# Kernel tuning notes

Measured on AMD Instinct MI355X. Metric: run time of the kernel, lower is better.

The kernel has to match this reference:

```python
import jax, jax.numpy as jnp
import numpy as np

K_HOP = 2

def _graph_conv(x, A, W, b):
    feats = [x]
    xk = x
    for _ in range(K_HOP):
        xk = jnp.einsum('bmn,bnc->bmc', A, xk)
        feats.append(xk)
    return jnp.concatenate(feats, -1) @ W + b

def _pair_mlp(y, W2, b2, W1, b1, shape):
    # normal_conv: fc1(relu(fc2(y))).reshape(shape)
    return (jax.nn.relu(y @ W2 + b2) @ W1 + b1).reshape(shape)

def setup_inputs():
    key = jax.random.key(0)
    ks = jax.random.split(key, 16)
    B, T, N = 8, 12, 200
    C_IN, H, D, H_ST = 2, 64, 32, 64
    def lin(k, fi, fo):
        k1, k2 = jax.random.split(k)
        s = 1.0 / float(np.sqrt(fi))
        return (jax.random.uniform(k1, (fi, fo), jnp.float32, -s, s),
                jax.random.uniform(k2, (fo,), jnp.float32, -s, s))
    W_s2d, b_s2d = lin(ks[0], H_ST, D)
    W_rz, b_rz = lin(ks[1], 1 + D, 2 * D)
    W_h, b_h = lin(ks[2], 1 + D, D)
    Wc2, bc2 = lin(ks[3], 2 * D, D)
    Wc1, bc1 = lin(ks[4], D, 1)
    Wm2, bm2 = lin(ks[5], 2 * D, D)
    Wm1, bm1 = lin(ks[6], D, 1)
    gin = (C_IN + H) * (1 + K_HOP)
    W_ru, b_ru = lin(ks[7], gin, 2 * H)
    W_cand, b_cand = lin(ks[8], gin, H)
    Wp1, bp1 = lin(ks[9], H, H)
    Wp2, bp2 = lin(ks[10], H, 1)
    x = jax.random.normal(ks[11], (B, T, N, C_IN), jnp.float32)
    node_fea_st = jax.random.normal(ks[12], (N, H_ST), jnp.float32)
    return dict(x=x, node_fea_st=node_fea_st, W_s2d=W_s2d, b_s2d=b_s2d,
                W_rz=W_rz, b_rz=b_rz, W_h=W_h, b_h=b_h,
                Wc2=Wc2, bc2=bc2, Wc1=Wc1, bc1=bc1,
                Wm2=Wm2, bm2=bm2, Wm1=Wm1, bm1=bm1,
                W_ru=W_ru, b_ru=b_ru, W_cand=W_cand, b_cand=b_cand,
                Wp1=Wp1, bp1=bp1, Wp2=Wp2, bp2=bp2)

def reference(x, node_fea_st, W_s2d, b_s2d, W_rz, b_rz, W_h, b_h,
              Wc2, bc2, Wc1, bc1, Wm2, bm2, Wm1, bm1,
              W_ru, b_ru, W_cand, b_cand, Wp1, bp1, Wp2, bp2):
    B, T, N, _ = x.shape
    H = W_cand.shape[1]
    D = W_h.shape[1]
    # states_dy init: linear_s2d(node_fea_st) broadcast over batch
    state_dy0 = jnp.broadcast_to((node_fea_st @ W_s2d + b_s2d)[None], (B, N, D))
    state0 = jnp.zeros((B, N, H), x.dtype)
    xs = jnp.transpose(x, (1, 0, 2, 3))  # [T,B,N,C]

    def step(carry, xt):
        state, state_dy = carry
        inp1 = xt[..., :1]
        # DynamicGraphGRU (conv_method='normal')
        rz = jax.nn.sigmoid(jnp.concatenate([inp1, state_dy], -1) @ W_rz + b_rz)
        r, z = jnp.split(rz, 2, -1)
        h = jnp.tanh(jnp.concatenate([inp1, r * state_dy], -1) @ W_h + b_h)
        new_dy = z * state_dy + (1.0 - z) * h
        s = jax.nn.relu(new_dy)  # [B,N,D]
        y = jnp.concatenate([jnp.broadcast_to(s[:, :, None, :], (B, N, N, D)),
                             jnp.broadcast_to(s[:, None, :, :], (B, N, N, D))], -1)
        g = _pair_mlp(y, Wc2, bc2, Wc1, bc1, (B, N, N))
        m = _pair_mlp(y, Wm2, bm2, Wm1, bm1, (B, N, N))
        A = g * jax.nn.sigmoid(m)  # dynamic graph [B,N,N]
        # DCGRUCell with supports=[A]
        ru = jax.nn.sigmoid(_graph_conv(jnp.concatenate([xt, state], -1), A, W_ru, b_ru))
        rr, u = jnp.split(ru, 2, -1)
        c = jnp.tanh(_graph_conv(jnp.concatenate([xt, rr * state], -1), A, W_cand, b_cand))
        new_state = u * state + (1.0 - u) * c
        return (new_state, new_dy), A

    (state, _), dy_graphs = jax.lax.scan(step, (state0, state_dy0), xs)
    # predictor: Linear -> LeakyReLU -> Linear
    pred = jax.nn.leaky_relu(state @ Wp1 + bp1) @ Wp2 + bp2  # [B,N,1]
    return pred, dy_graphs
```

## Files before the change

kernel.cpp:

```cpp
#include <hip/hip_runtime.h>
#include <math.h>

#define B_ 8
#define T_ 12
#define N_ 200
#define R_ 1600
#define NN_ 40000

__device__ __forceinline__ float sigm(float v) { return 1.f / (1.f + expf(-v)); }

__global__ void __launch_bounds__(256) k_dyall(
        const float* __restrict__ x,  const float* __restrict__ nf,
        const float* __restrict__ Ws2d, const float* __restrict__ bs2d,
        const float* __restrict__ Wrz,  const float* __restrict__ brz,
        const float* __restrict__ Wh,   const float* __restrict__ bh,
        const float* __restrict__ Wc2,  const float* __restrict__ Wm2,
        const float* __restrict__ bc2,  const float* __restrict__ bm2,
        float* __restrict__ Pc, float* __restrict__ Qc,
        float* __restrict__ Pm, float* __restrict__ Qm,
        float* __restrict__ state) {
    __shared__ float sWs2d[64 * 32], sWrz[33 * 64], sWh[33 * 32];
    __shared__ float sWc2[64 * 32], sWm2[64 * 32];
    __shared__ float sbrz[64], sbh[32], sbs2d[32], sbc2[32], sbm2[32];
    __shared__ float nfs[4][64], dy[4][32], in1[4][33], in2[4][33], rz[4][64], s4[4][32];
    int bk = blockIdx.x, tid = threadIdx.x;
    int w = tid >> 6, o = tid & 63;
    int row = bk * 4 + w, b = row / N_, n = row % N_;
    state[bk * 256 + tid] = 0.f;
    for (int idx = tid; idx < 2048; idx += 256) sWs2d[idx] = Ws2d[idx];
    for (int idx = tid; idx < 2112; idx += 256) sWrz[idx] = Wrz[idx];
    for (int idx = tid; idx < 1056; idx += 256) sWh[idx] = Wh[idx];
    for (int idx = tid; idx < 2048; idx += 256) { sWc2[idx] = Wc2[idx]; sWm2[idx] = Wm2[idx]; }
    if (tid < 64) sbrz[tid] = brz[tid];
    if (tid < 32) { sbh[tid] = bh[tid]; sbs2d[tid] = bs2d[tid];
                    sbc2[tid] = bc2[tid]; sbm2[tid] = bm2[tid]; }
    nfs[w][o] = nf[n * 64 + o];
    __syncthreads();
    if (o < 32) {
        float acc = sbs2d[o];
        #pragma unroll 8
        for (int i = 0; i < 64; ++i) acc += nfs[w][i] * sWs2d[i * 32 + o];
        dy[w][o] = acc;
    }
    __syncthreads();
    for (int t = 0; t < T_; ++t) {
        if (o == 0) { float v = x[((b * T_ + t) * N_ + n) * 2]; in1[w][0] = v; in2[w][0] = v; }
        if (o < 32) in1[w][o + 1] = dy[w][o];
        __syncthreads();
        float acc = sbrz[o];
        #pragma unroll
        for (int i = 0; i < 33; ++i) acc += in1[w][i] * sWrz[i * 64 + o];
        rz[w][o] = sigm(acc);
        __syncthreads();
        if (o < 32) in2[w][o + 1] = rz[w][o] * dy[w][o];
        __syncthreads();
        if (o < 32) {
            float h = sbh[o];
            #pragma unroll
            for (int i = 0; i < 33; ++i) h += in2[w][i] * sWh[i * 32 + o];
            h = tanhf(h);
            float z = rz[w][32 + o];
            float nd = z * dy[w][o] + (1.f - z) * h;
            dy[w][o] = nd;
            s4[w][o] = nd > 0.f ? nd : 0.f;
        }
        __syncthreads();
        size_t base = ((size_t)t * R_ + row) * 32;
        for (int idx = o; idx < 128; idx += 64) {
            int mat = idx >> 5, k = idx & 31;
            const float* W = (mat < 2) ? sWc2 : sWm2;
            int rb = (mat & 1) ? 32 : 0;
            float a = (mat == 0) ? sbc2[k] : (mat == 2) ? sbm2[k] : 0.f;
            #pragma unroll
            for (int i = 0; i < 32; ++i) a += s4[w][i] * W[(rb + i) * 32 + k];
            ((mat == 0) ? Pc : (mat == 1) ? Qc : (mat == 2) ? Pm : Qm)[base + k] = a;
        }
        __syncthreads();
    }
}

__global__ void __launch_bounds__(256) k_pairall(
        const float* __restrict__ Pc, const float* __restrict__ Qc,
        const float* __restrict__ Pm, const float* __restrict__ Qm,
        const float* __restrict__ Wc1, const float* __restrict__ bc1,
        const float* __restrict__ Wm1, const float* __restrict__ bm1,
        float* __restrict__ out) {
    __shared__ float sPc[16][36], sQc[16][36], sPm[16][36], sQm[16][36];
    __shared__ float sWc1[32], sWm1[32];
    int z = blockIdx.z;
    int i0 = blockIdx.x * 16, j0 = blockIdx.y * 16;
    int tid = threadIdx.y * 16 + threadIdx.x;
    size_t tb = (size_t)z * N_;
    for (int l = tid; l < 128; l += 256) {
        int r = l >> 3, q = l & 7;
        int gi = i0 + r, gj = j0 + r;
        float4 z4 = make_float4(0.f, 0.f, 0.f, 0.f);
        *(float4*)&sPc[r][4 * q] = (gi < N_) ? *(const float4*)&Pc[(tb + gi) * 32 + 4 * q] : z4;
        *(float4*)&sPm[r][4 * q] = (gi < N_) ? *(const float4*)&Pm[(tb + gi) * 32 + 4 * q] : z4;
        *(float4*)&sQc[r][4 * q] = (gj < N_) ? *(const float4*)&Qc[(tb + gj) * 32 + 4 * q] : z4;
        *(float4*)&sQm[r][4 * q] = (gj < N_) ? *(const float4*)&Qm[(tb + gj) * 32 + 4 * q] : z4;
    }
    if (tid < 32) { sWc1[tid] = Wc1[tid]; sWm1[tid] = Wm1[tid]; }
    __syncthreads();
    int i = i0 + threadIdx.y, j = j0 + threadIdx.x;
    if (i >= N_ || j >= N_) return;
    int ty = threadIdx.y, tx = threadIdx.x;
    float g0 = 0.f, g1 = 0.f, m0 = 0.f, m1 = 0.f;
    #pragma unroll
    for (int kg = 0; kg < 8; ++kg) {
        float4 pc = *(const float4*)&sPc[ty][4 * kg];
        float4 qc = *(const float4*)&sQc[tx][4 * kg];
        float4 wc = *(const float4*)&sWc1[4 * kg];
        g0 += fmaxf(pc.x + qc.x, 0.f) * wc.x + fmaxf(pc.y + qc.y, 0.f) * wc.y;
        g1 += fmaxf(pc.z + qc.z, 0.f) * wc.z + fmaxf(pc.w + qc.w, 0.f) * wc.w;
        float4 pm = *(const float4*)&sPm[ty][4 * kg];
        float4 qm = *(const float4*)&sQm[tx][4 * kg];
        float4 wm = *(const float4*)&sWm1[4 * kg];
        m0 += fmaxf(pm.x + qm.x, 0.f) * wm.x + fmaxf(pm.y + qm.y, 0.f) * wm.y;
        m1 += fmaxf(pm.z + qm.z, 0.f) * wm.z + fmaxf(pm.w + qm.w, 0.f) * wm.w;
    }
    float g = g0 + g1 + bc1[0];
    float m = m0 + m1 + bm1[0];
    out[R_ + (((size_t)z * N_ + i) * N_ + j)] = g * sigm(m);
}

__global__ void __launch_bounds__(256) k_a2(
        const float* __restrict__ Abase, float* __restrict__ Cbase, int nmat) {
    __shared__ float Ast[32][132];
    __shared__ float Bs[32][68];
    int bx = blockIdx.x;
    int z = bx % nmat, tl = bx / nmat;
    int i0 = (tl >> 2) * 128, j0 = (tl & 3) * 64;
    const float* Az = Abase + (size_t)z * NN_;
    float* Cz = Cbase + (size_t)z * NN_;
    int tid = threadIdx.x;
    int tx = tid & 15, ty = tid >> 4;
    float acc[8][4] = {};
    for (int k0 = 0; k0 < 200; k0 += 32) {
        {
            int i = tid >> 1;
            int kb = (tid & 1) * 16;
            int gi = i0 + i;
            #pragma unroll
            for (int q = 0; q < 4; ++q) {
                int k = kb + q * 4;
                int gk = k0 + k;
                float4 v = make_float4(0.f, 0.f, 0.f, 0.f);
                if (gi < N_) {
                    if (gk + 3 < N_) v = *(const float4*)&Az[gi * N_ + gk];
                    else {
                        float t0 = (gk + 0 < N_) ? Az[gi * N_ + gk + 0] : 0.f;
                        float t1 = (gk + 1 < N_) ? Az[gi * N_ + gk + 1] : 0.f;
                        float t2 = (gk + 2 < N_) ? Az[gi * N_ + gk + 2] : 0.f;
                        float t3 = (gk + 3 < N_) ? Az[gi * N_ + gk + 3] : 0.f;
                        v = make_float4(t0, t1, t2, t3);
                    }
                }
                Ast[k + 0][i] = v.x; Ast[k + 1][i] = v.y;
                Ast[k + 2][i] = v.z; Ast[k + 3][i] = v.w;
            }
        }
        {
            #pragma unroll
            for (int q = 0; q < 2; ++q) {
                int id = tid + 256 * q;
                int k = id >> 4, jq = (id & 15) * 4;
                int gk = k0 + k, gj = j0 + jq;
                float4 v = make_float4(0.f, 0.f, 0.f, 0.f);
                if (gk < N_) {
                    if (gj + 3 < N_) v = *(const float4*)&Az[gk * N_ + gj];
                    else {
                        float t0 = (gj + 0 < N_) ? Az[gk * N_ + gj + 0] : 0.f;
                        float t1 = (gj + 1 < N_) ? Az[gk * N_ + gj + 1] : 0.f;
                        float t2 = (gj + 2 < N_) ? Az[gk * N_ + gj + 2] : 0.f;
                        float t3 = (gj + 3 < N_) ? Az[gk * N_ + gj + 3] : 0.f;
                        v = make_float4(t0, t1, t2, t3);
                    }
                }
                *(float4*)&Bs[k][jq] = v;
            }
        }
        __syncthreads();
        #pragma unroll 8
        for (int k = 0; k < 32; ++k) {
            float4 a0 = *(const float4*)&Ast[k][ty * 8];
            float4 a1 = *(const float4*)&Ast[k][ty * 8 + 4];
            float4 bv = *(const float4*)&Bs[k][tx * 4];
            acc[0][0] += a0.x * bv.x; acc[0][1] += a0.x * bv.y; acc[0][2] += a0.x * bv.z; acc[0][3] += a0.x * bv.w;
            acc[1][0] += a0.y * bv.x; acc[1][1] += a0.y * bv.y; acc[1][2] += a0.y * bv.z; acc[1][3] += a0.y * bv.w;
            acc[2][0] += a0.z * bv.x; acc[2][1] += a0.z * bv.y; acc[2][2] += a0.z * bv.z; acc[2][3] += a0.z * bv.w;
            acc[3][0] += a0.w * bv.x; acc[3][1] += a0.w * bv.y; acc[3][2] += a0.w * bv.z; acc[3][3] += a0.w * bv.w;
            acc[4][0] += a1.x * bv.x; acc[4][1] += a1.x * bv.y; acc[4][2] += a1.x * bv.z; acc[4][3] += a1.x * bv.w;
            acc[5][0] += a1.y * bv.x; acc[5][1] += a1.y * bv.y; acc[5][2] += a1.y * bv.z; acc[5][3] += a1.y * bv.w;
            acc[6][0] += a1.z * bv.x; acc[6][1] += a1.z * bv.y; acc[6][2] += a1.z * bv.z; acc[6][3] += a1.z * bv.w;
            acc[7][0] += a1.w * bv.x; acc[7][1] += a1.w * bv.y; acc[7][2] += a1.w * bv.z; acc[7][3] += a1.w * bv.w;
        }
        __syncthreads();
    }
    #pragma unroll
    for (int r = 0; r < 8; ++r) {
        int gi = i0 + ty * 8 + r;
        if (gi >= N_) continue;
        int gj = j0 + tx * 4;
        if (gj + 3 < N_) {
            *(float4*)&Cz[gi * N_ + gj] = make_float4(acc[r][0], acc[r][1], acc[r][2], acc[r][3]);
        } else {
            #pragma unroll
            for (int e = 0; e < 4; ++e) if (gj + e < N_) Cz[gi * N_ + gj + e] = acc[r][e];
        }
    }
}

__global__ void __launch_bounds__(256) k_xh(
        const float* __restrict__ Abase, const float* __restrict__ A2base,
        const float* __restrict__ x, int z0, float* __restrict__ xh) {
    __shared__ float xtl[400];
    int zl = blockIdx.x, tid = threadIdx.x;
    int z = z0 + zl, t = z >> 3, b = z & 7;
    int w = tid >> 6, l = tid & 63;
    const float* xb = x + ((size_t)(b * T_ + t)) * N_ * 2;
    for (int idx = tid; idx < 400; idx += 256) xtl[idx] = xb[idx];
    __syncthreads();
    for (int it = 0; it < 50; ++it) {
        int i = it * 4 + w;
        float p0 = 0.f, p1 = 0.f, p2 = 0.f, p3 = 0.f;
        if (l < 50) {
            float4 a4 = *(const float4*)(Abase + (size_t)zl * NN_ + i * 200 + 4 * l);
            float4 c4 = *(const float4*)(A2base + (size_t)zl * NN_ + i * 200 + 4 * l);
            #pragma unroll
            for (int q = 0; q < 4; ++q) {
                float av = (&a4.x)[q], cv = (&c4.x)[q];
                float x0 = xtl[(4 * l + q) * 2], x1 = xtl[(4 * l + q) * 2 + 1];
                p0 += av * x0; p1 += av * x1; p2 += cv * x0; p3 += cv * x1;
            }
        }
        #pragma unroll
        for (int off = 32; off > 0; off >>= 1) {
            p0 += __shfl_down(p0, off); p1 += __shfl_down(p1, off);
            p2 += __shfl_down(p2, off); p3 += __shfl_down(p3, off);
        }
        if (l == 0) *(float4*)(xh + ((size_t)zl * N_ + i) * 4) = make_float4(p0, p1, p2, p3);
    }
}

__global__ void __launch_bounds__(256) k_ru2(
        const float* __restrict__ At, const float* __restrict__ A2t,
        const float* __restrict__ xht,
        const float* __restrict__ x, int t, const float* __restrict__ state,
        const float* __restrict__ Wru, const float* __restrict__ bru,
        float* __restrict__ rs, float* __restrict__ ub) {
    __shared__ float a2s[2 * 200], c2s[2 * 200];
    __shared__ float hpA[4][64], hpC[4][64];
    __shared__ float g8[2][132];
    __shared__ float xts[4];
    int bx = blockIdx.x;
    int b = bx & 7, i0 = (bx >> 3) * 2;
    int tid = threadIdx.x;
    const float* F = state + (size_t)b * (N_ * 64);
    {
        const float4* Ar = (const float4*)(At + ((size_t)b * N_ + i0) * 200);
        const float4* Cr = (const float4*)(A2t + ((size_t)b * N_ + i0) * 200);
        if (tid < 100) { ((float4*)a2s)[tid] = Ar[tid]; ((float4*)c2s)[tid] = Cr[tid]; }
        if (tid >= 128 && tid < 132) {
            int l = tid - 128;
            xts[l] = x[((size_t)(b * T_ + t) * N_ + i0 + (l >> 1)) * 2 + (l & 1)];
        }
        if (tid >= 136 && tid < 144) {
            int l = tid - 136, rr = l >> 2, q = l & 3;
            g8[rr][(q < 2) ? q : q + 64] = xht[((size_t)b * N_ + i0 + rr) * 4 + q];
        }
    }
    __syncthreads();
    {
        int w = tid >> 6, lane = tid & 63;
        int r = w & 1, h = w >> 1;
        int cg = lane & 15, jq = lane >> 4;
        const float* ar = a2s + r * 200 + h * 100;
        const float* cr = c2s + r * 200 + h * 100;
        const float* Fb = F + (size_t)(h * 100) * 64 + 4 * cg;
        float4 accA = make_float4(0.f, 0.f, 0.f, 0.f);
        float4 accC = make_float4(0.f, 0.f, 0.f, 0.f);
        #pragma unroll 5
        for (int m = 0; m < 25; ++m) {
            int j = jq + 4 * m;
            float av = ar[j], cv = cr[j];
            float4 f4 = *(const float4*)&Fb[(size_t)j * 64];
            accA.x += av * f4.x; accA.y += av * f4.y; accA.z += av * f4.z; accA.w += av * f4.w;
            accC.x += cv * f4.x; accC.y += cv * f4.y; accC.z += cv * f4.z; accC.w += cv * f4.w;
        }
        accA.x += __shfl_xor(accA.x, 16); accA.y += __shfl_xor(accA.y, 16);
        accA.z += __shfl_xor(accA.z, 16); accA.w += __shfl_xor(accA.w, 16);
        accC.x += __shfl_xor(accC.x, 16); accC.y += __shfl_xor(accC.y, 16);
        accC.z += __shfl_xor(accC.z, 16); accC.w += __shfl_xor(accC.w, 16);
        accA.x += __shfl_xor(accA.x, 32); accA.y += __shfl_xor(accA.y, 32);
        accA.z += __shfl_xor(accA.z, 32); accA.w += __shfl_xor(accA.w, 32);
        accC.x += __shfl_xor(accC.x, 32); accC.y += __shfl_xor(accC.y, 32);
        accC.z += __shfl_xor(accC.z, 32); accC.w += __shfl_xor(accC.w, 32);
        if (lane < 16) {
            *(float4*)&hpA[w][4 * cg] = accA;
            *(float4*)&hpC[w][4 * cg] = accC;
        }
    }
    __syncthreads();
    {
        int mt = tid >> 7, r = (tid >> 6) & 1, c = tid & 63;
        float v = mt ? (hpC[r][c] + hpC[2 + r][c]) : (hpA[r][c] + hpA[2 + r][c]);
        g8[r][(mt ? 68 : 2) + c] = v;
    }
    __syncthreads();
    {
        int rq = tid >> 7, c = tid & 127;
        int grow = i0 + rq;
        const float* Fr = F + (size_t)grow * 64;
        float a0 = bru[c] + xts[rq * 2 + 0] * Wru[c] + xts[rq * 2 + 1] * Wru[128 + c];
        #pragma unroll 4
        for (int kg = 0; kg < 16; ++kg) {
            float4 f0 = *(const float4*)&Fr[4 * kg];
            const float* Wp = Wru + (size_t)(2 + 4 * kg) * 128 + c;
            a0 += f0.x * Wp[0] + f0.y * Wp[128] + f0.z * Wp[256] + f0.w * Wp[384];
        }
        #pragma unroll 4
        for (int kg = 0; kg < 33; ++kg) {
            float4 f0 = *(const float4*)&g8[rq][4 * kg];
            const float* Wp = Wru + (size_t)(66 + 4 * kg) * 128 + c;
            a0 += f0.x * Wp[0] + f0.y * Wp[128] + f0.z * Wp[256] + f0.w * Wp[384];
        }
        float v = sigm(a0);
        size_t go = (size_t)b * N_ + grow;
        if (c < 64) rs[go * 64 + c] = v * Fr[c];
        else        ub[go * 64 + (c - 64)] = v;
    }
}

__global__ void __launch_bounds__(256) k_cand2(
        const float* __restrict__ At, const float* __restrict__ A2t,
        const float* __restrict__ xht,
        const float* __restrict__ x, int t, const float* __restrict__ rsin,
        const float* __restrict__ Wcd, const float* __restrict__ bcd,
        const float* __restrict__ ub, float* __restrict__ state) {
    __shared__ float a2s[2 * 200], c2s[2 * 200];
    __shared__ float hpA[4][64], hpC[4][64];
    __shared__ float g8[2][132];
    __shared__ float xts[4];
    __shared__ float gp[2][2][64];
    int bx = blockIdx.x;
    int b = bx & 7, i0 = (bx >> 3) * 2;
    int tid = threadIdx.x;
    const float* F = rsin + (size_t)b * (N_ * 64);
    {
        const float4* Ar = (const float4*)(At + ((size_t)b * N_ + i0) * 200);
        const float4* Cr = (const float4*)(A2t + ((size_t)b * N_ + i0) * 200);
        if (tid < 100) { ((float4*)a2s)[tid] = Ar[tid]; ((float4*)c2s)[tid] = Cr[tid]; }
        if (tid >= 128 && tid < 132) {
            int l = tid - 128;
            xts[l] = x[((size_t)(b * T_ + t) * N_ + i0 + (l >> 1)) * 2 + (l & 1)];
        }
        if (tid >= 136 && tid < 144) {
            int l = tid - 136, rr = l >> 2, q = l & 3;
            g8[rr][(q < 2) ? q : q + 64] = xht[((size_t)b * N_ + i0 + rr) * 4 + q];
        }
    }
    __syncthreads();
    {
        int w = tid >> 6, lane = tid & 63;
        int r = w & 1, h = w >> 1;
        int cg = lane & 15, jq = lane >> 4;
        const float* ar = a2s + r * 200 + h * 100;
        const float* cr = c2s + r * 200 + h * 100;
        const float* Fb = F + (size_t)(h * 100) * 64 + 4 * cg;
        float4 accA = make_float4(0.f, 0.f, 0.f, 0.f);
        float4 accC = make_float4(0.f, 0.f, 0.f, 0.f);
        #pragma unroll 5
        for (int m = 0; m < 25; ++m) {
            int j = jq + 4 * m;
            float av = ar[j], cv = cr[j];
            float4 f4 = *(const float4*)&Fb[(size_t)j * 64];
            accA.x += av * f4.x; accA.y += av * f4.y; accA.z += av * f4.z; accA.w += av * f4.w;
            accC.x += cv * f4.x; accC.y += cv * f4.y; accC.z += cv * f4.z; accC.w += cv * f4.w;
        }
        accA.x += __shfl_xor(accA.x, 16); accA.y += __shfl_xor(accA.y, 16);
        accA.z += __shfl_xor(accA.z, 16); accA.w += __shfl_xor(accA.w, 16);
        accC.x += __shfl_xor(accC.x, 16); accC.y += __shfl_xor(accC.y, 16);
        accC.z += __shfl_xor(accC.z, 16); accC.w += __shfl_xor(accC.w, 16);
        accA.x += __shfl_xor(accA.x, 32); accA.y += __shfl_xor(accA.y, 32);
        accA.z += __shfl_xor(accA.z, 32); accA.w += __shfl_xor(accA.w, 32);
        accC.x += __shfl_xor(accC.x, 32); accC.y += __shfl_xor(accC.y, 32);
        accC.z += __shfl_xor(accC.z, 32); accC.w += __shfl_xor(accC.w, 32);
        if (lane < 16) {
            *(float4*)&hpA[w][4 * cg] = accA;
            *(float4*)&hpC[w][4 * cg] = accC;
        }
    }
    __syncthreads();
    {
        int mt = tid >> 7, r = (tid >> 6) & 1, c = tid & 63;
        float v = mt ? (hpC[r][c] + hpC[2 + r][c]) : (hpA[r][c] + hpA[2 + r][c]);
        g8[r][(mt ? 68 : 2) + c] = v;
    }
    __syncthreads();
    {
        int kh = tid >> 7, rq = (tid >> 6) & 1, c = tid & 63;
        int grow = i0 + rq;
        const float* Fr = F + (size_t)grow * 64;
        float a0 = 0.f;
        if (kh == 0) {
            a0 = bcd[c] + xts[rq * 2 + 0] * Wcd[c] + xts[rq * 2 + 1] * Wcd[64 + c];
            #pragma unroll 4
            for (int kg = 0; kg < 16; ++kg) {
                float4 f0 = *(const float4*)&Fr[4 * kg];
                const float* Wp = Wcd + (size_t)(2 + 4 * kg) * 64 + c;
                a0 += f0.x * Wp[0] + f0.y * Wp[64] + f0.z * Wp[128] + f0.w * Wp[192];
            }
            #pragma unroll 4
            for (int kg = 0; kg < 8; ++kg) {
                float4 f0 = *(const float4*)&g8[rq][4 * kg];
                const float* Wp = Wcd + (size_t)(66 + 4 * kg) * 64 + c;
                a0 += f0.x * Wp[0] + f0.y * Wp[64] + f0.z * Wp[128] + f0.w * Wp[192];
            }
        } else {
            #pragma unroll 5
            for (int kg = 8; kg < 33; ++kg) {
                float4 f0 = *(const float4*)&g8[rq][4 * kg];
                const float* Wp = Wcd + (size_t)(66 + 4 * kg) * 64 + c;
                a0 += f0.x * Wp[0] + f0.y * Wp[64] + f0.z * Wp[128] + f0.w * Wp[192];
            }
        }
        gp[kh][rq][c] = a0;
    }
    __syncthreads();
    if (tid < 128) {
        int rq = tid >> 6, c = tid & 63;
        size_t go = (size_t)b * N_ + i0 + rq;
        float a = gp[0][rq][c] + gp[1][rq][c];
        float cnd = tanhf(a);
        float u = ub[go * 64 + c];
        float st = state[go * 64 + c];
        state[go * 64 + c] = u * st + (1.f - u) * cnd;
    }
}

__global__ void __launch_bounds__(64) k_pred(
        const float* __restrict__ state,
        const float* __restrict__ Wp1, const float* __restrict__ bp1,
        const float* __restrict__ Wp2, const float* __restrict__ bp2,
        float* __restrict__ out) {
    __shared__ float st[64];
    int row = blockIdx.x;
    int tid = threadIdx.x;
    st[tid] = state[row * 64 + tid];
    __syncthreads();
    float acc = bp1[tid];
    #pragma unroll 8
    for (int a = 0; a < 64; ++a) acc += st[a] * Wp1[a * 64 + tid];
    acc = acc > 0.f ? acc : 0.01f * acc;
    float v = acc * Wp2[tid];
    #pragma unroll
    for (int off = 32; off > 0; off >>= 1) v += __shfl_down(v, off);
    if (tid == 0) out[row] = v + bp2[0];
}

extern "C" void kernel_launch(void* const* d_in, const int* in_sizes, int n_in,
                              void* d_out, int out_size, void* d_ws, size_t ws_size,
                              hipStream_t stream) {
    const float* x    = (const float*)d_in[0];
    const float* nf   = (const float*)d_in[1];
    const float* Ws2d = (const float*)d_in[2];
    const float* bs2d = (const float*)d_in[3];
    const float* Wrz  = (const float*)d_in[4];
    const float* brz  = (const float*)d_in[5];
    const float* Wh   = (const float*)d_in[6];
    const float* bh   = (const float*)d_in[7];
    const float* Wc2  = (const float*)d_in[8];
    const float* bc2  = (const float*)d_in[9];
    const float* Wc1  = (const float*)d_in[10];
    const float* bc1  = (const float*)d_in[11];
    const float* Wm2  = (const float*)d_in[12];
    const float* bm2  = (const float*)d_in[13];
    const float* Wm1  = (const float*)d_in[14];
    const float* bm1  = (const float*)d_in[15];
    const float* Wru  = (const float*)d_in[16];
    const float* bru  = (const float*)d_in[17];
    const float* Wcand= (const float*)d_in[18];
    const float* bcand= (const float*)d_in[19];
    const float* Wp1  = (const float*)d_in[20];
    const float* bp1  = (const float*)d_in[21];
    const float* Wp2  = (const float*)d_in[22];
    const float* bp2  = (const float*)d_in[23];
    float* out = (float*)d_out;

    float* ws = (float*)d_ws;
    const size_t PQ = (size_t)T_ * R_ * 32;
    float* Pc = ws;
    float* Qc = Pc + PQ;
    float* Pm = Qc + PQ;
    float* Qm = Pm + PQ;

    const size_t A2F = (size_t)96 * NN_;
    const size_t XHF = (size_t)96 * N_ * 4;
    const size_t FULL_NEED = (A2F + XHF + 3 * (size_t)R_ * 64) * 4;
    bool full = ws_size >= FULL_NEED;

    const float* Aall = out + R_;

    if (full) {
        float* A2base = ws;
        float* xhbase = ws + A2F;
        float* state  = xhbase + XHF;
        float* rs     = state + (size_t)R_ * 64;
        float* ub     = rs + (size_t)R_ * 64;

        k_dyall<<<400, 256, 0, stream>>>(x, nf, Ws2d, bs2d, Wrz, brz, Wh, bh,
                                         Wc2, Wm2, bc2, bm2, Pc, Qc, Pm, Qm, state);
        k_pairall<<<dim3(13, 13, 96), dim3(16, 16), 0, stream>>>(
            Pc, Qc, Pm, Qm, Wc1, bc1, Wm1, bm1, out);
        k_a2<<<96 * 8, 256, 0, stream>>>(Aall, A2base, 96);
        k_xh<<<96, 256, 0, stream>>>(Aall, A2base, x, 0, xhbase);

        for (int t = 0; t < T_; ++t) {
            const float* At  = Aall + (size_t)t * 8 * NN_;
            const float* A2t = A2base + (size_t)t * 8 * NN_;
            const float* xht = xhbase + (size_t)t * 8 * N_ * 4;
            k_ru2  <<<800, 256, 0, stream>>>(At, A2t, xht, x, t, state, Wru, bru, rs, ub);
            k_cand2<<<800, 256, 0, stream>>>(At, A2t, xht, x, t, rs, Wcand, bcand, ub, state);
        }
        k_pred<<<R_, 64, 0, stream>>>(state, Wp1, bp1, Wp2, bp2, out);
    } else {
        float* A2base = ws + 4 * PQ;
        float* xhbase = A2base + (size_t)8 * NN_;
        float* state  = xhbase + (size_t)8 * N_ * 4;
        float* rs     = state + (size_t)R_ * 64;
        float* ub     = rs + (size_t)R_ * 64;

        k_dyall<<<400, 256, 0, stream>>>(x, nf, Ws2d, bs2d, Wrz, brz, Wh, bh,
                                         Wc2, Wm2, bc2, bm2, Pc, Qc, Pm, Qm, state);
        k_pairall<<<dim3(13, 13, 96), dim3(16, 16), 0, stream>>>(
            Pc, Qc, Pm, Qm, Wc1, bc1, Wm1, bm1, out);
        for (int t = 0; t < T_; ++t) {
            const float* At = Aall + (size_t)t * 8 * NN_;
            k_a2<<<8 * 8, 256, 0, stream>>>(At, A2base, 8);
            k_xh<<<8, 256, 0, stream>>>(At, A2base, x, t * 8, xhbase);
            k_ru2  <<<800, 256, 0, stream>>>(At, A2base, xhbase, x, t, state, Wru, bru, rs, ub);
            k_cand2<<<800, 256, 0, stream>>>(At, A2base, xhbase, x, t, rs, Wcand, bcand, ub, state);
        }
        k_pred<<<R_, 64, 0, stream>>>(state, Wp1, bp1, Wp2, bp2, out);
    }
}
```

Measured before the change: 550.8 us.

## Split gate linear layers across K with shared feature staging and float4 weight loads

The ru and candidate kernels now build a contiguous 198-wide feature row per node in shared memory (x, state, A·F, A²·F) instead of mixing global and shared reads. The output linear is then split along the reduction dimension across thread groups, with each thread loading float4 weight vectors and computing both rows, followed by a shared-memory partial-sum reduction. This replaces long serial per-thread dot products with strided scalar weight loads, aiming to cut latency and reuse each weight load for two rows. In exchange it adds an extra barrier, more shared memory, and a partial-sum reduction step.

```diff
diff --git a/kernel.cpp b/kernel.cpp
--- a/kernel.cpp
+++ b/kernel.cpp
@@ -251,8 +251,8 @@
         float* __restrict__ rs, float* __restrict__ ub) {
     __shared__ float a2s[2 * 200], c2s[2 * 200];
     __shared__ float hpA[4][64], hpC[4][64];
-    __shared__ float g8[2][132];
-    __shared__ float xts[4];
+    __shared__ float feat[2][200];
+    __shared__ float gp[8][2][128];
     int bx = blockIdx.x;
     int b = bx & 7, i0 = (bx >> 3) * 2;
     int tid = threadIdx.x;
@@ -261,13 +261,17 @@
         const float4* Ar = (const float4*)(At + ((size_t)b * N_ + i0) * 200);
         const float4* Cr = (const float4*)(A2t + ((size_t)b * N_ + i0) * 200);
         if (tid < 100) { ((float4*)a2s)[tid] = Ar[tid]; ((float4*)c2s)[tid] = Cr[tid]; }
-        if (tid >= 128 && tid < 132) {
-            int l = tid - 128;
-            xts[l] = x[((size_t)(b * T_ + t) * N_ + i0 + (l >> 1)) * 2 + (l & 1)];
-        }
-        if (tid >= 136 && tid < 144) {
-            int l = tid - 136, rr = l >> 2, q = l & 3;
-            g8[rr][(q < 2) ? q : q + 64] = xht[((size_t)b * N_ + i0 + rr) * 4 + q];
+        if (tid >= 100 && tid < 164) {
+            int l = tid - 100, r = l >> 5, q = l & 31;
+            *(float2*)&feat[r][2 + 2 * q] = *(const float2*)&F[(size_t)(i0 + r) * 64 + 2 * q];
+        }
+        if (tid >= 164 && tid < 168) {
+            int l = tid - 164;
+            feat[l >> 1][l & 1] = x[((size_t)(b * T_ + t) * N_ + i0 + (l >> 1)) * 2 + (l & 1)];
+        }
+        if (tid >= 168 && tid < 176) {
+            int l = tid - 168, rr = l >> 2, q = l & 3;
+            feat[rr][(q < 2) ? (66 + q) : (132 + q - 2)] = xht[((size_t)b * N_ + i0 + rr) * 4 + q];
         }
     }
     __syncthreads();
@@ -305,29 +309,32 @@
     {
         int mt = tid >> 7, r = (tid >> 6) & 1, c = tid & 63;
         float v = mt ? (hpC[r][c] + hpC[2 + r][c]) : (hpA[r][c] + hpA[2 + r][c]);
-        g8[r][(mt ? 68 : 2) + c] = v;
+        feat[r][(mt ? 134 : 68) + c] = v;
+    }
+    __syncthreads();
+    {
+        int cq = tid & 31, kh = tid >> 5;
+        int k0 = 25 * kh, kend = (k0 + 25 < 198) ? (k0 + 25) : 198;
+        float4 s0 = make_float4(0.f, 0.f, 0.f, 0.f);
+        float4 s1 = make_float4(0.f, 0.f, 0.f, 0.f);
+        for (int k = k0; k < kend; ++k) {
+            float4 w4 = *(const float4*)&Wru[(size_t)k * 128 + 4 * cq];
+            float f0 = feat[0][k], f1 = feat[1][k];
+            s0.x += f0 * w4.x; s0.y += f0 * w4.y; s0.z += f0 * w4.z; s0.w += f0 * w4.w;
+            s1.x += f1 * w4.x; s1.y += f1 * w4.y; s1.z += f1 * w4.z; s1.w += f1 * w4.w;
+        }
+        *(float4*)&gp[kh][0][4 * cq] = s0;
+        *(float4*)&gp[kh][1][4 * cq] = s1;
     }
     __syncthreads();
     {
         int rq = tid >> 7, c = tid & 127;
-        int grow = i0 + rq;
-        const float* Fr = F + (size_t)grow * 64;
-        float a0 = bru[c] + xts[rq * 2 + 0] * Wru[c] + xts[rq * 2 + 1] * Wru[128 + c];
-        #pragma unroll 4
-        for (int kg = 0; kg < 16; ++kg) {
-            float4 f0 = *(const float4*)&Fr[4 * kg];
-            const float* Wp = Wru + (size_t)(2 + 4 * kg) * 128 + c;
-            a0 += f0.x * Wp[0] + f0.y * Wp[128] + f0.z * Wp[256] + f0.w * Wp[384];
-        }
-        #pragma unroll 4
-        for (int kg = 0; kg < 33; ++kg) {
-            float4 f0 = *(const float4*)&g8[rq][4 * kg];
-            const float* Wp = Wru + (size_t)(66 + 4 * kg) * 128 + c;
-            a0 += f0.x * Wp[0] + f0.y * Wp[128] + f0.z * Wp[256] + f0.w * Wp[384];
-        }
-        float v = sigm(a0);
-        size_t go = (size_t)b * N_ + grow;
-        if (c < 64) rs[go * 64 + c] = v * Fr[c];
+        float a = bru[c];
+        #pragma unroll
+        for (int h = 0; h < 8; ++h) a += gp[h][rq][c];
+        float v = sigm(a);
+        size_t go = (size_t)b * N_ + i0 + rq;
+        if (c < 64) rs[go * 64 + c] = v * feat[rq][2 + c];
         else        ub[go * 64 + (c - 64)] = v;
     }
 }
@@ -340,9 +347,8 @@
         const float* __restrict__ ub, float* __restrict__ state) {
     __shared__ float a2s[2 * 200], c2s[2 * 200];
     __shared__ float hpA[4][64], hpC[4][64];
-    __shared__ float g8[2][132];
-    __shared__ float xts[4];
-    __shared__ float gp[2][2][64];
+    __shared__ float feat[2][200];
+    __shared__ float gp[16][2][64];
     int bx = blockIdx.x;
     int b = bx & 7, i0 = (bx >> 3) * 2;
     int tid = threadIdx.x;
@@ -351,13 +357,17 @@
         const float4* Ar = (const float4*)(At + ((size_t)b * N_ + i0) * 200);
         const float4* Cr = (const float4*)(A2t + ((size_t)b * N_ + i0) * 200);
         if (tid < 100) { ((float4*)a2s)[tid] = Ar[tid]; ((float4*)c2s)[tid] = Cr[tid]; }
-        if (tid >= 128 && tid < 132) {
-            int l = tid - 128;
-            xts[l] = x[((size_t)(b * T_ + t) * N_ + i0 + (l >> 1)) * 2 + (l & 1)];
-        }
-        if (tid >= 136 && tid < 144) {
-            int l = tid - 136, rr = l >> 2, q = l & 3;
-            g8[rr][(q < 2) ? q : q + 64] = xht[((size_t)b * N_ + i0 + rr) * 4 + q];
+        if (tid >= 100 && tid < 164) {
+            int l = tid - 100, r = l >> 5, q = l & 31;
+            *(float2*)&feat[r][2 + 2 * q] = *(const float2*)&F[(size_t)(i0 + r) * 64 + 2 * q];
+        }
+        if (tid >= 164 && tid < 168) {
+            int l = tid - 164;
+            feat[l >> 1][l & 1] = x[((size_t)(b * T_ + t) * N_ + i0 + (l >> 1)) * 2 + (l & 1)];
+        }
+        if (tid >= 168 && tid < 176) {
+            int l = tid - 168, rr = l >> 2, q = l & 3;
+            feat[rr][(q < 2) ? (66 + q) : (132 + q - 2)] = xht[((size_t)b * N_ + i0 + rr) * 4 + q];
         }
     }
     __syncthreads();
@@ -395,43 +405,30 @@
     {
         int mt = tid >> 7, r = (tid >> 6) & 1, c = tid & 63;
         float v = mt ? (hpC[r][c] + hpC[2 + r][c]) : (hpA[r][c] + hpA[2 + r][c]);
-        g8[r][(mt ? 68 : 2) + c] = v;
-    }
-    __syncthreads();
-    {
-        int kh = tid >> 7, rq = (tid >> 6) & 1, c = tid & 63;
-        int grow = i0 + rq;
-        const float* Fr = F + (size_t)grow * 64;
-        float a0 = 0.f;
-        if (kh == 0) {
-            a0 = bcd[c] + xts[rq * 2 + 0] * Wcd[c] + xts[rq * 2 + 1] * Wcd[64 + c];
-            #pragma unroll 4
-            for (int kg = 0; kg < 16; ++kg) {
-                float4 f0 = *(const float4*)&Fr[4 * kg];
-                const float* Wp = Wcd + (size_t)(2 + 4 * kg) * 64 + c;
-                a0 += f0.x * Wp[0] + f0.y * Wp[64] + f0.z * Wp[128] + f0.w * Wp[192];
-            }
-            #pragma unroll 4
-            for (int kg = 0; kg < 8; ++kg) {
-                float4 f0 = *(const float4*)&g8[rq][4 * kg];
-                const float* Wp = Wcd + (size_t)(66 + 4 * kg) * 64 + c;
-                a0 += f0.x * Wp[0] + f0.y * Wp[64] + f0.z * Wp[128] + f0.w * Wp[192];
-            }
-        } else {
-            #pragma unroll 5
-            for (int kg = 8; kg < 33; ++kg) {
-                float4 f0 = *(const float4*)&g8[rq][4 * kg];
-                const float* Wp = Wcd + (size_t)(66 + 4 * kg) * 64 + c;
-                a0 += f0.x * Wp[0] + f0.y * Wp[64] + f0.z * Wp[128] + f0.w * Wp[192];
-            }
-        }
-        gp[kh][rq][c] = a0;
+        feat[r][(mt ? 134 : 68) + c] = v;
+    }
+    __syncthreads();
+    {
+        int cq = tid & 15, kh = tid >> 4;
+        int k0 = 13 * kh, kend = (k0 + 13 < 198) ? (k0 + 13) : 198;
+        float4 s0 = make_float4(0.f, 0.f, 0.f, 0.f);
+        float4 s1 = make_float4(0.f, 0.f, 0.f, 0.f);
+        for (int k = k0; k < kend; ++k) {
+            float4 w4 = *(const float4*)&Wcd[(size_t)k * 64 + 4 * cq];
+            float f0 = feat[0][k], f1 = feat[1][k];
+            s0.x += f0 * w4.x; s0.y += f0 * w4.y; s0.z += f0 * w4.z; s0.w += f0 * w4.w;
+            s1.x += f1 * w4.x; s1.y += f1 * w4.y; s1.z += f1 * w4.z; s1.w += f1 * w4.w;
+        }
+        *(float4*)&gp[kh][0][4 * cq] = s0;
+        *(float4*)&gp[kh][1][4 * cq] = s1;
     }
     __syncthreads();
     if (tid < 128) {
         int rq = tid >> 6, c = tid & 63;
+        float a = bcd[c];
+        #pragma unroll
+        for (int h = 0; h < 16; ++h) a += gp[h][rq][c];
         size_t go = (size_t)b * N_ + i0 + rq;
-        float a = gp[0][rq][c] + gp[1][rq][c];
         float cnd = tanhf(a);
         float u = ub[go * 64 + c];
         float st = state[go * 64 + c];
```

After: 477.4 us. 1.15x faster.
